# Optimization experiments

Measured on AMD Instinct MI355X. Metric: run time of the kernel, lower is better.

Reference implementation:

```python
import jax, jax.numpy as jnp
import numpy as np

N, IN_FEATS, OUT_FEATS = 8192, 512, 256


def setup_inputs() -> dict:
    key = jax.random.key(0)
    k1, k2, k3, k4 = jax.random.split(key, 4)
    feature_mat = jax.random.normal(k1, (N, IN_FEATS), dtype=jnp.float32)
    # Xavier-uniform style init for W and W2
    limW = float(np.sqrt(6.0 / (IN_FEATS + OUT_FEATS)))
    W = jax.random.uniform(k2, (IN_FEATS, OUT_FEATS), minval=-limW, maxval=limW, dtype=jnp.float32)
    limW2 = float(np.sqrt(6.0 / (2 * OUT_FEATS + 1)))
    W2 = jax.random.uniform(k3, (2 * OUT_FEATS, 1), minval=-limW2, maxval=limW2, dtype=jnp.float32)
    adj_mat = jax.random.randint(k4, (N, N), 0, 2, dtype=jnp.int32)
    return {"feature_mat": feature_mat, "W": W, "W2": W2, "adj_mat": adj_mat}


def reference(feature_mat, W, W2, adj_mat):
    out_feats = W.shape[1]
    Wh = feature_mat @ W                      # [N, F']
    Wh1 = Wh @ W2[:out_feats, :]              # [N, 1]
    Wh2 = Wh @ W2[out_feats:, :]              # [N, 1]
    e = Wh1 + Wh2.T                           # [N, N] broadcast add
    e = jnp.where(e > 0, e, 0.2 * e)          # leaky_relu(0.2)
    # NOTE: original masks with ZERO (not -inf) before softmax — faithful.
    e = jnp.where(adj_mat > 0, e, jnp.zeros((), dtype=e.dtype))
    attention = jax.nn.softmax(e, axis=1)     # row softmax over all N
    h_prime = attention @ Wh                  # [N, F']
    return jax.nn.relu(h_prime)
```

## Files before the change

kernel.cpp:

```cpp
#include <hip/hip_runtime.h>
#include <cstdint>
#include <cstddef>

#define NR 8192
#define FOUT 256
#define KIN 512
#define KSPLIT 2
#define JCHUNK (NR / KSPLIT)
#define BKJ 64
#define NSTEP (JCHUNK / BKJ)
#define IROWS 32

typedef __attribute__((ext_vector_type(8))) short bf16x8;
typedef __attribute__((ext_vector_type(4))) float f32x4;

__device__ __forceinline__ unsigned f2bf(float x) {
  unsigned u = __float_as_uint(x);
  u += 0x7fffu + ((u >> 16) & 1u);
  return u >> 16;
}
__device__ __forceinline__ float bf2f(unsigned h) {
  return __uint_as_float(h << 16);
}
__device__ __forceinline__ unsigned fkey(float x) {
  unsigned u = __float_as_uint(x);
  return (u & 0x80000000u) ? ~u : (u | 0x80000000u);
}
__device__ __forceinline__ float fkey_dec(unsigned k) {
  return __uint_as_float((k & 0x80000000u) ? (k ^ 0x80000000u) : ~k);
}

#define GLDS(g, l)                                                            \
  __builtin_amdgcn_global_load_lds(                                           \
      (const __attribute__((address_space(1))) unsigned int*)(g),             \
      (__attribute__((address_space(3))) unsigned int*)(l), 16, 0, 0)

__global__ __launch_bounds__(256) void k0_prep(const float* __restrict__ W,
                                               const float* __restrict__ W2,
                                               float* __restrict__ w1,
                                               float* __restrict__ w2,
                                               char* __restrict__ WTbf,
                                               unsigned* __restrict__ maxkey) {
  if (blockIdx.x == 0 && threadIdx.x == 0) *maxkey = 0u;
  int wv = threadIdx.x >> 6, lane = threadIdx.x & 63;
  int k = blockIdx.x * 4 + wv;
  int f4 = lane * 4;
  float4 wr = *(const float4*)(W + (size_t)k * FOUT + f4);
  float4 a = *(const float4*)(W2 + f4);
  float4 b = *(const float4*)(W2 + FOUT + f4);
  float d1 = wr.x * a.x + wr.y * a.y + wr.z * a.z + wr.w * a.w;
  float d2 = wr.x * b.x + wr.y * b.y + wr.z * b.z + wr.w * b.w;
#pragma unroll
  for (int off = 32; off; off >>= 1) {
    d1 += __shfl_xor(d1, off);
    d2 += __shfl_xor(d2, off);
  }
  if (lane == 0) {
    w1[k] = d1;
    w2[k] = d2;
  }
  int kt = k >> 5, kl = k & 31;
  float wv4[4] = {wr.x, wr.y, wr.z, wr.w};
#pragma unroll
  for (int ff = 0; ff < 4; ++ff) {
    int f = f4 + ff;
    size_t addr = (size_t)kt * 16384 + (f >> 4) * 1024 +
                  (((f & 15) | (((kl >> 3) & 3) << 4)) * 16) + (kl & 7) * 2;
    *(unsigned short*)(WTbf + addr) = (unsigned short)f2bf(wv4[ff]);
  }
}

__global__ __launch_bounds__(256) void k2_fused(
    const float* __restrict__ X, const char* __restrict__ WTbf,
    const float* __restrict__ w1, const float* __restrict__ w2,
    char* __restrict__ WhTf, float* __restrict__ Wh1, float* __restrict__ Wh2,
    unsigned* __restrict__ maxkey) {
  __shared__ char smem[2 * 18432 + 4096];
  char* buf0 = smem;
  char* buf1 = smem + 18432;
  char* wlds = smem + 2 * 18432;
  int t = threadIdx.x, wv = t >> 6, lane = t & 63;
  int jb = blockIdx.x * 32;
  int jr = t >> 3, koff = (t & 7) * 4;
  int cA = (jr & 15) | (((koff >> 3) & 3) << 4);
  int swA = cA ^ (((cA >> 4) & 3) << 2);
  int aoff = (jr >> 4) * 1024 + swA * 16 + ((koff & 4) << 1);
  int slotR = lane ^ (((lane >> 4) & 3) << 2);
  const float* xrow = X + (size_t)(jb + jr) * KIN + koff;

  {
    float2 a_ = *(const float2*)(w1 + t * 2);
    float2 b_ = *(const float2*)(w2 + t * 2);
    *(float2*)(wlds + t * 8) = a_;
    *(float2*)(wlds + 2048 + t * 8) = b_;
  }
  __syncthreads();

  float4 st0, st1, st2, st3;
  float d1 = 0.f, d2 = 0.f;
  f32x4 acc[2][4];
#pragma unroll
  for (int a = 0; a < 2; ++a)
#pragma unroll
    for (int b = 0; b < 4; ++b) acc[a][b] = (f32x4){0.f, 0.f, 0.f, 0.f};

#define K2_GLB(KT, BUFW)                                                      \
  do {                                                                        \
    const char* gs_ = WTbf + ((size_t)(KT) << 14) + (wv << 12) + lane * 16;   \
    char* ld_ = (BUFW) + 2048 + (wv << 12);                                   \
    GLDS(gs_, ld_);                                                           \
    GLDS(gs_ + 1024, ld_ + 1024);                                             \
    GLDS(gs_ + 2048, ld_ + 2048);                                             \
    GLDS(gs_ + 3072, ld_ + 3072);                                             \
  } while (0)

#define K2_LDX(KT, ST) (ST) = *(const float4*)(xrow + (KT) * 32)

#define K2_AGEN(ST, BUFW, SNUM)                                               \
  do {                                                                        \
    uint2 a_;                                                                 \
    a_.x = f2bf((ST).x) | (f2bf((ST).y) << 16);                               \
    a_.y = f2bf((ST).z) | (f2bf((ST).w) << 16);                               \
    *(uint2*)((BUFW) + aoff) = a_;                                            \
    float4 wa_ = *(const float4*)(wlds + ((SNUM)*32 + koff) * 4);             \
    float4 wb_ = *(const float4*)(wlds + 2048 + ((SNUM)*32 + koff) * 4);      \
    d1 += (ST).x * wa_.x + (ST).y * wa_.y + (ST).z * wa_.z + (ST).w * wa_.w;  \
    d2 += (ST).x * wb_.x + (ST).y * wb_.y + (ST).z * wb_.z + (ST).w * wb_.w;  \
  } while (0)

#define K2_ITER(S, BUFR, BUFW, STC, STF)                                      \
  do {                                                                        \
    int s_ = (S);                                                             \
    if (s_ + 1 < 16) K2_GLB(s_ + 1, BUFW);                                    \
    K2_LDX((s_ + 3 < 16) ? s_ + 3 : 15, STF);                                 \
    if (s_ + 1 < 16) K2_AGEN(STC, BUFW, s_ + 1);                              \
    bf16x8 a0 = *(const bf16x8*)((BUFR) + slotR * 16);                        \
    bf16x8 a1 = *(const bf16x8*)((BUFR) + 1024 + slotR * 16);                 \
    bf16x8 b0 = *(const bf16x8*)((BUFR) + 2048 + (wv * 4 + 0) * 1024 + lane * 16); \
    bf16x8 b1 = *(const bf16x8*)((BUFR) + 2048 + (wv * 4 + 1) * 1024 + lane * 16); \
    bf16x8 b2 = *(const bf16x8*)((BUFR) + 2048 + (wv * 4 + 2) * 1024 + lane * 16); \
    bf16x8 b3 = *(const bf16x8*)((BUFR) + 2048 + (wv * 4 + 3) * 1024 + lane * 16); \
    acc[0][0] = __builtin_amdgcn_mfma_f32_16x16x32_bf16(a0, b0, acc[0][0], 0, 0, 0); \
    acc[0][1] = __builtin_amdgcn_mfma_f32_16x16x32_bf16(a0, b1, acc[0][1], 0, 0, 0); \
    acc[0][2] = __builtin_amdgcn_mfma_f32_16x16x32_bf16(a0, b2, acc[0][2], 0, 0, 0); \
    acc[0][3] = __builtin_amdgcn_mfma_f32_16x16x32_bf16(a0, b3, acc[0][3], 0, 0, 0); \
    acc[1][0] = __builtin_amdgcn_mfma_f32_16x16x32_bf16(a1, b0, acc[1][0], 0, 0, 0); \
    acc[1][1] = __builtin_amdgcn_mfma_f32_16x16x32_bf16(a1, b1, acc[1][1], 0, 0, 0); \
    acc[1][2] = __builtin_amdgcn_mfma_f32_16x16x32_bf16(a1, b2, acc[1][2], 0, 0, 0); \
    acc[1][3] = __builtin_amdgcn_mfma_f32_16x16x32_bf16(a1, b3, acc[1][3], 0, 0, 0); \
    __builtin_amdgcn_sched_barrier(0);                                        \
    asm volatile("s_waitcnt vmcnt(1)");                                       \
    asm volatile("s_waitcnt lgkmcnt(0)");                                     \
    __builtin_amdgcn_s_barrier();                                             \
    __builtin_amdgcn_sched_barrier(0);                                        \
  } while (0)

  K2_GLB(0, buf0);
  K2_LDX(0, st0);
  K2_LDX(1, st1);
  K2_LDX(2, st2);
  K2_AGEN(st0, buf0, 0);
  __builtin_amdgcn_sched_barrier(0);
  asm volatile("s_waitcnt vmcnt(2)");
  asm volatile("s_waitcnt lgkmcnt(0)");
  __builtin_amdgcn_s_barrier();
  __builtin_amdgcn_sched_barrier(0);

  for (int s4 = 0; s4 < 16; s4 += 4) {
    K2_ITER(s4 + 0, buf0, buf1, st1, st3);
    K2_ITER(s4 + 1, buf1, buf0, st2, st0);
    K2_ITER(s4 + 2, buf0, buf1, st3, st1);
    K2_ITER(s4 + 3, buf1, buf0, st0, st2);
  }
#undef K2_ITER
#undef K2_AGEN
#undef K2_LDX
#undef K2_GLB

  int q = lane >> 4;
#pragma unroll
  for (int mi = 0; mi < 2; ++mi)
#pragma unroll
    for (int nn = 0; nn < 4; ++nn) {
      int u2 = wv * 4 + nn;
      int cell = (lane & 15) | ((((mi * 2) + (q >> 1)) & 3) << 4);
      uint2 v;
      v.x = f2bf(acc[mi][nn].x) | (f2bf(acc[mi][nn].y) << 16);
      v.y = f2bf(acc[mi][nn].z) | (f2bf(acc[mi][nn].w) << 16);
      *(uint2*)(buf0 + 2048 + u2 * 1024 + cell * 16 + ((q & 1) << 3)) = v;
    }
  __syncthreads();
  char* wb = WhTf + (size_t)blockIdx.x * 16384;
#pragma unroll
  for (int q2 = 0; q2 < 4; ++q2) {
    uint4 v = *(const uint4*)(buf0 + 2048 + q2 * 4096 + t * 16);
    *(uint4*)(wb + q2 * 4096 + t * 16) = v;
  }

  d1 += __shfl_xor(d1, 1);
  d1 += __shfl_xor(d1, 2);
  d1 += __shfl_xor(d1, 4);
  d2 += __shfl_xor(d2, 1);
  d2 += __shfl_xor(d2, 2);
  d2 += __shfl_xor(d2, 4);
  if ((t & 7) == 0) {
    Wh1[jb + jr] = d1;
    Wh2[jb + jr] = d2;
  }
  float mx = d2;
#pragma unroll
  for (int off = 32; off >= 8; off >>= 1) mx = fmaxf(mx, __shfl_xor(mx, off));
  __shared__ float red[4];
  if (lane == 0) red[wv] = mx;
  __syncthreads();
  if (t == 0) {
    float bm = fmaxf(fmaxf(red[0], red[1]), fmaxf(red[2], red[3]));
    atomicMax(maxkey, fkey(bm));
  }
}

__device__ __forceinline__ uint2 hv4(int4 aq, float4 wq, float wh1, float m,
                                     float enm, float& z) {
  float s0 = wh1 + wq.x, s1 = wh1 + wq.y, s2 = wh1 + wq.z, s3 = wh1 + wq.w;
  s0 = s0 > 0.f ? s0 : 0.2f * s0;
  s1 = s1 > 0.f ? s1 : 0.2f * s1;
  s2 = s2 > 0.f ? s2 : 0.2f * s2;
  s3 = s3 > 0.f ? s3 : 0.2f * s3;
  float w0 = aq.x > 0 ? __expf(s0 - m) : enm;
  float w1 = aq.y > 0 ? __expf(s1 - m) : enm;
  float w2 = aq.z > 0 ? __expf(s2 - m) : enm;
  float w3 = aq.w > 0 ? __expf(s3 - m) : enm;
  unsigned h0 = f2bf(w0), h1 = f2bf(w1), h2 = f2bf(w2), h3 = f2bf(w3);
  z += bf2f(h0) + bf2f(h1) + bf2f(h2) + bf2f(h3);
  uint2 r;
  r.x = h0 | (h1 << 16);
  r.y = h2 | (h3 << 16);
  return r;
}

__global__ __launch_bounds__(512, 4) void k3_attn(
    const int* __restrict__ adj, const char* __restrict__ WhTf,
    const float* __restrict__ Wh1, const float* __restrict__ Wh2,
    const unsigned* __restrict__ maxptr, float* __restrict__ PVp,
    float* __restrict__ Zp) {
  __shared__ char smem[24576];
  char* abuf0 = smem;
  char* abuf1 = smem + 4096;
  char* wlds = smem + 8192;
  int t = threadIdx.x, wv = t >> 6, lane = t & 63;
  int kc = blockIdx.x & 1;
  int ib = blockIdx.x >> 1;
  int ibase = ib * IROWS;
  int jbch = kc * JCHUNK;
  int r0 = t >> 4;
  int jg = (t & 15) * 4;
  int iglob = ibase + r0;
  float maxwh2 = fkey_dec(*maxptr);
  float wh1 = Wh1[iglob];
  float m = fmaxf(0.f, wh1 + maxwh2);
  float enm = __expf(-m);
  int cA = (r0 & 15) | (((jg >> 3) & 3) << 4);
  int swA = cA ^ (((cA >> 4) & 3) << 2);
  int aoff = ((r0 >> 4) * 2 + (jg >> 5)) * 1024 + swA * 16 + ((jg & 4) << 1);
  int slotR = lane ^ (((lane >> 4) & 3) << 2);
  const int* adjrow = adj + ((size_t)iglob << 13) + jbch + jg;
  const char* bbase = WhTf + ((size_t)(kc * 128) << 14) + (size_t)(wv * 2) * 1024 +
                      (size_t)lane * 16;
  const char* wl = wlds + ((t & 15) << 4);

  {
    const float* wp = Wh2 + jbch + t * 8;
    *(float4*)(wlds + t * 32) = *(const float4*)(wp);
    *(float4*)(wlds + t * 32 + 16) = *(const float4*)(wp + 4);
  }
  __syncthreads();

  int4 st0, st1, st2, st3;
  bf16x8 bA0, bA1, bA2, bA3, bB0, bB1, bB2, bB3;
  f32x4 acc[2][2];
#pragma unroll
  for (int a = 0; a < 2; ++a)
#pragma unroll
    for (int b = 0; b < 2; ++b) acc[a][b] = (f32x4){0.f, 0.f, 0.f, 0.f};
  float zacc = 0.f;

#define K3_LDB(S, B0, B1, B2, B3)                                             \
  do {                                                                        \
    int sc_ = (S) < NSTEP ? (S) : NSTEP - 1;                                  \
    const char* bp_ = bbase + (size_t)(2 * sc_) * 16384;                      \
    B0 = *(const bf16x8*)(bp_);                                               \
    B1 = *(const bf16x8*)(bp_ + 1024);                                        \
    B2 = *(const bf16x8*)(bp_ + 16384);                                       \
    B3 = *(const bf16x8*)(bp_ + 16384 + 1024);                                \
  } while (0)

#define K3_LDA(S, ST)                                                         \
  do {                                                                        \
    int sc_ = (S) < NSTEP ? (S) : NSTEP - 1;                                  \
    ST = *(const int4*)(adjrow + sc_ * BKJ);                                  \
  } while (0)

#define K3_ITER(S, AR, AW, BC0, BC1, BC2, BC3, BF0, BF1, BF2, BF3, STC, STF,  \
                DO_HV)                                                        \
  do {                                                                        \
    int s_ = (S);                                                             \
    K3_LDB(s_ + 1, BF0, BF1, BF2, BF3);                                       \
    K3_LDA(s_ + 4, STF);                                                      \
    if (DO_HV) {                                                              \
      float4 wq_ = *(const float4*)(wl + (s_ + 1) * 256);                     \
      uint2 a_ = hv4(STC, wq_, wh1, m, enm, zacc);                            \
      *(uint2*)((AW) + aoff) = a_;                                            \
    }                                                                         \
    bf16x8 a00 = *(const bf16x8*)((AR) + 0 * 1024 + slotR * 16);              \
    bf16x8 a10 = *(const bf16x8*)((AR) + 2 * 1024 + slotR * 16);              \
    bf16x8 a01 = *(const bf16x8*)((AR) + 1 * 1024 + slotR * 16);              \
    bf16x8 a11 = *(const bf16x8*)((AR) + 3 * 1024 + slotR * 16);              \
    acc[0][0] = __builtin_amdgcn_mfma_f32_16x16x32_bf16(a00, BC0, acc[0][0], 0, 0, 0); \
    acc[0][1] = __builtin_amdgcn_mfma_f32_16x16x32_bf16(a00, BC1, acc[0][1], 0, 0, 0); \
    acc[1][0] = __builtin_amdgcn_mfma_f32_16x16x32_bf16(a10, BC0, acc[1][0], 0, 0, 0); \
    acc[1][1] = __builtin_amdgcn_mfma_f32_16x16x32_bf16(a10, BC1, acc[1][1], 0, 0, 0); \
    acc[0][0] = __builtin_amdgcn_mfma_f32_16x16x32_bf16(a01, BC2, acc[0][0], 0, 0, 0); \
    acc[0][1] = __builtin_amdgcn_mfma_f32_16x16x32_bf16(a01, BC3, acc[0][1], 0, 0, 0); \
    acc[1][0] = __builtin_amdgcn_mfma_f32_16x16x32_bf16(a11, BC2, acc[1][0], 0, 0, 0); \
    acc[1][1] = __builtin_amdgcn_mfma_f32_16x16x32_bf16(a11, BC3, acc[1][1], 0, 0, 0); \
    __builtin_amdgcn_sched_barrier(0);                                        \
    asm volatile("s_waitcnt lgkmcnt(0)" ::: "memory");                        \
    __builtin_amdgcn_s_barrier();                                             \
    __builtin_amdgcn_sched_barrier(0);                                        \
  } while (0)

  K3_LDB(0, bA0, bA1, bA2, bA3);
  int4 adj0;
  K3_LDA(0, adj0);
  K3_LDA(1, st1);
  K3_LDA(2, st2);
  K3_LDA(3, st3);
  {
    float4 wq0 = *(const float4*)(wl);
    uint2 a0 = hv4(adj0, wq0, wh1, m, enm, zacc);
    *(uint2*)(abuf0 + aoff) = a0;
  }
  __builtin_amdgcn_sched_barrier(0);
  asm volatile("s_waitcnt lgkmcnt(0)" ::: "memory");
  __builtin_amdgcn_s_barrier();
  __builtin_amdgcn_sched_barrier(0);

  for (int s4 = 0; s4 < NSTEP - 4; s4 += 4) {
    K3_ITER(s4 + 0, abuf0, abuf1, bA0, bA1, bA2, bA3, bB0, bB1, bB2, bB3, st1, st0, 1);
    K3_ITER(s4 + 1, abuf1, abuf0, bB0, bB1, bB2, bB3, bA0, bA1, bA2, bA3, st2, st1, 1);
    K3_ITER(s4 + 2, abuf0, abuf1, bA0, bA1, bA2, bA3, bB0, bB1, bB2, bB3, st3, st2, 1);
    K3_ITER(s4 + 3, abuf1, abuf0, bB0, bB1, bB2, bB3, bA0, bA1, bA2, bA3, st0, st3, 1);
  }
  K3_ITER(NSTEP - 4, abuf0, abuf1, bA0, bA1, bA2, bA3, bB0, bB1, bB2, bB3, st1, st0, 1);
  K3_ITER(NSTEP - 3, abuf1, abuf0, bB0, bB1, bB2, bB3, bA0, bA1, bA2, bA3, st2, st1, 1);
  K3_ITER(NSTEP - 2, abuf0, abuf1, bA0, bA1, bA2, bA3, bB0, bB1, bB2, bB3, st3, st2, 1);
  K3_ITER(NSTEP - 1, abuf1, abuf0, bB0, bB1, bB2, bB3, bA0, bA1, bA2, bA3, st0, st3, 0);
#undef K3_ITER
#undef K3_LDA
#undef K3_LDB

  zacc += __shfl_xor(zacc, 1);
  zacc += __shfl_xor(zacc, 2);
  zacc += __shfl_xor(zacc, 4);
  zacc += __shfl_xor(zacc, 8);
  if ((t & 15) == 0) Zp[(size_t)kc * NR + iglob] = zacc;
#pragma unroll
  for (int rf = 0; rf < 2; ++rf)
#pragma unroll
    for (int un = 0; un < 2; ++un) {
      int f = wv * 32 + un * 16 + (lane & 15);
      int row0 = ibase + rf * 16 + ((lane >> 4) << 2);
      size_t base = ((size_t)kc * NR + row0) * FOUT + f;
      PVp[base + 0 * FOUT] = acc[rf][un].x;
      PVp[base + 1 * FOUT] = acc[rf][un].y;
      PVp[base + 2 * FOUT] = acc[rf][un].z;
      PVp[base + 3 * FOUT] = acc[rf][un].w;
    }
}

__global__ __launch_bounds__(256) void k4_reduce(const float* __restrict__ PVp,
                                                 const float* __restrict__ Zp,
                                                 float* __restrict__ out) {
  int tid = blockIdx.x * 256 + threadIdx.x;
  int i = tid >> 6;
  int f4 = (tid & 63) * 4;
  float z = Zp[i] + Zp[NR + i];
  float4 p0 = *(const float4*)(PVp + (size_t)i * FOUT + f4);
  float4 p1 = *(const float4*)(PVp + ((size_t)NR + i) * FOUT + f4);
  float inv = 1.f / z;
  float4 r;
  r.x = fmaxf((p0.x + p1.x) * inv, 0.f);
  r.y = fmaxf((p0.y + p1.y) * inv, 0.f);
  r.z = fmaxf((p0.z + p1.z) * inv, 0.f);
  r.w = fmaxf((p0.w + p1.w) * inv, 0.f);
  *(float4*)(out + (size_t)i * FOUT + f4) = r;
}

extern "C" void kernel_launch(void* const* d_in, const int* in_sizes, int n_in,
                              void* d_out, int out_size, void* d_ws,
                              size_t ws_size, hipStream_t stream) {
  const float* X = (const float*)d_in[0];
  const float* W = (const float*)d_in[1];
  const float* W2 = (const float*)d_in[2];
  const int* adj = (const int*)d_in[3];
  float* out = (float*)d_out;
  char* ws = (char*)d_ws;

  const size_t WHT_OFF = 0;
  const size_t WTBF_OFF = (size_t)4 * 1024 * 1024;
  const size_t W1_OFF = WTBF_OFF + 256 * 1024;
  const size_t W2V_OFF = W1_OFF + 2048;
  const size_t WH1_OFF = W2V_OFF + 2048;
  const size_t WH2_OFF = WH1_OFF + 32768;
  const size_t MXK_OFF = WH2_OFF + 32768;
  const size_t ZP_OFF = MXK_OFF + 256;
  const size_t PV_OFF = ZP_OFF + (size_t)KSPLIT * NR * 4;

  char* WhTf = ws + WHT_OFF;
  char* WTbf = ws + WTBF_OFF;
  float* w1 = (float*)(ws + W1_OFF);
  float* w2 = (float*)(ws + W2V_OFF);
  float* Wh1 = (float*)(ws + WH1_OFF);
  float* Wh2 = (float*)(ws + WH2_OFF);
  unsigned* maxkey = (unsigned*)(ws + MXK_OFF);
  float* Zp = (float*)(ws + ZP_OFF);
  float* PVp = (float*)(ws + PV_OFF);

  k0_prep<<<128, 256, 0, stream>>>(W, W2, w1, w2, WTbf, maxkey);
  k2_fused<<<256, 256, 0, stream>>>(X, WTbf, w1, w2, WhTf, Wh1, Wh2, maxkey);
  k3_attn<<<512, 512, 0, stream>>>(adj, WhTf, Wh1, Wh2, maxkey, PVp, Zp);
  k4_reduce<<<2048, 256, 0, stream>>>(PVp, Zp, out);
}
```

Measured before the change: 130.4 us.

## Double row tile and split columns four ways in attention kernel

Raises the attention block's row tile from 32 to 64 rows and the column split from 2 to 4 chunks. Each thread now builds 8 probability values per step, and each wave runs 4x2 MFMA tiles per step, so every bf16 Wh B-fragment loaded from global memory is reused across twice as many rows. The adjacency prefetch depth shrinks from 4 stages to 2. The reduce kernel now sums four partial products, which doubles the partial-output traffic written and read.

```diff
diff --git a/kernel.cpp b/kernel.cpp
--- a/kernel.cpp
+++ b/kernel.cpp
@@ -5,11 +5,11 @@
 #define NR 8192
 #define FOUT 256
 #define KIN 512
-#define KSPLIT 2
+#define KSPLIT 4
 #define JCHUNK (NR / KSPLIT)
 #define BKJ 64
 #define NSTEP (JCHUNK / BKJ)
-#define IROWS 32
+#define IROWS 64
 
 typedef __attribute__((ext_vector_type(8))) short bf16x8;
 typedef __attribute__((ext_vector_type(4))) float f32x4;
@@ -237,6 +237,12 @@
   r.y = h2 | (h3 << 16);
   return r;
 }
+__device__ __forceinline__ uint4 hv8(int4 a0, int4 a1, float4 w0, float4 w1,
+                                     float wh1, float m, float enm, float& z) {
+  uint2 r0 = hv4(a0, w0, wh1, m, enm, z);
+  uint2 r1 = hv4(a1, w1, wh1, m, enm, z);
+  return (uint4){r0.x, r0.y, r1.x, r1.y};
+}
 
 __global__ __launch_bounds__(512, 4) void k3_attn(
     const int* __restrict__ adj, const char* __restrict__ WhTf,
@@ -245,41 +251,38 @@
     float* __restrict__ Zp) {
   __shared__ char smem[24576];
   char* abuf0 = smem;
-  char* abuf1 = smem + 4096;
-  char* wlds = smem + 8192;
+  char* abuf1 = smem + 8192;
+  char* wlds = smem + 16384;
   int t = threadIdx.x, wv = t >> 6, lane = t & 63;
-  int kc = blockIdx.x & 1;
-  int ib = blockIdx.x >> 1;
+  int kc = blockIdx.x & 3;
+  int ib = blockIdx.x >> 2;
   int ibase = ib * IROWS;
   int jbch = kc * JCHUNK;
-  int r0 = t >> 4;
-  int jg = (t & 15) * 4;
+  int r0 = t >> 3;
+  int j8 = (t & 7) * 8;
   int iglob = ibase + r0;
   float maxwh2 = fkey_dec(*maxptr);
   float wh1 = Wh1[iglob];
   float m = fmaxf(0.f, wh1 + maxwh2);
   float enm = __expf(-m);
-  int cA = (r0 & 15) | (((jg >> 3) & 3) << 4);
+  int unitA = (r0 >> 4) * 2 + (j8 >> 5);
+  int cA = (r0 & 15) | (((j8 & 31) >> 3) << 4);
   int swA = cA ^ (((cA >> 4) & 3) << 2);
-  int aoff = ((r0 >> 4) * 2 + (jg >> 5)) * 1024 + swA * 16 + ((jg & 4) << 1);
+  int aoff = unitA * 1024 + swA * 16;
   int slotR = lane ^ (((lane >> 4) & 3) << 2);
-  const int* adjrow = adj + ((size_t)iglob << 13) + jbch + jg;
-  const char* bbase = WhTf + ((size_t)(kc * 128) << 14) + (size_t)(wv * 2) * 1024 +
-                      (size_t)lane * 16;
-  const char* wl = wlds + ((t & 15) << 4);
-
-  {
-    const float* wp = Wh2 + jbch + t * 8;
-    *(float4*)(wlds + t * 32) = *(const float4*)(wp);
-    *(float4*)(wlds + t * 32 + 16) = *(const float4*)(wp + 4);
-  }
+  const int* adjrow = adj + ((size_t)iglob << 13) + jbch + j8;
+  const char* bbase = WhTf + ((size_t)(kc * 64) << 14) +
+                      (size_t)(wv * 2) * 1024 + (size_t)lane * 16;
+  const char* wl = wlds + j8 * 4;
+
+  *(float4*)(wlds + t * 16) = *(const float4*)(Wh2 + jbch + t * 4);
   __syncthreads();
 
-  int4 st0, st1, st2, st3;
   bf16x8 bA0, bA1, bA2, bA3, bB0, bB1, bB2, bB3;
-  f32x4 acc[2][2];
-#pragma unroll
-  for (int a = 0; a < 2; ++a)
+  int4 st0_a, st0_b, st1_a, st1_b;
+  f32x4 acc[4][2];
+#pragma unroll
+  for (int a = 0; a < 4; ++a)
 #pragma unroll
     for (int b = 0; b < 2; ++b) acc[a][b] = (f32x4){0.f, 0.f, 0.f, 0.f};
   float zacc = 0.f;
@@ -297,32 +300,30 @@
 #define K3_LDA(S, ST)                                                         \
   do {                                                                        \
     int sc_ = (S) < NSTEP ? (S) : NSTEP - 1;                                  \
-    ST = *(const int4*)(adjrow + sc_ * BKJ);                                  \
-  } while (0)
-
-#define K3_ITER(S, AR, AW, BC0, BC1, BC2, BC3, BF0, BF1, BF2, BF3, STC, STF,  \
-                DO_HV)                                                        \
+    ST##_a = *(const int4*)(adjrow + sc_ * BKJ);                              \
+    ST##_b = *(const int4*)(adjrow + sc_ * BKJ + 4);                          \
+  } while (0)
+
+#define K3_ITER(S, AR, AW, BC0, BC1, BC2, BC3, BF0, BF1, BF2, BF3, STC, DO_HV) \
   do {                                                                        \
     int s_ = (S);                                                             \
     K3_LDB(s_ + 1, BF0, BF1, BF2, BF3);                                       \
-    K3_LDA(s_ + 4, STF);                                                      \
     if (DO_HV) {                                                              \
-      float4 wq_ = *(const float4*)(wl + (s_ + 1) * 256);                     \
-      uint2 a_ = hv4(STC, wq_, wh1, m, enm, zacc);                            \
-      *(uint2*)((AW) + aoff) = a_;                                            \
+      float4 wq0_ = *(const float4*)(wl + (s_ + 1) * 256);                    \
+      float4 wq1_ = *(const float4*)(wl + (s_ + 1) * 256 + 16);               \
+      uint4 a_ = hv8(STC##_a, STC##_b, wq0_, wq1_, wh1, m, enm, zacc);        \
+      *(uint4*)((AW) + aoff) = a_;                                            \
     }                                                                         \
-    bf16x8 a00 = *(const bf16x8*)((AR) + 0 * 1024 + slotR * 16);              \
-    bf16x8 a10 = *(const bf16x8*)((AR) + 2 * 1024 + slotR * 16);              \
-    bf16x8 a01 = *(const bf16x8*)((AR) + 1 * 1024 + slotR * 16);              \
-    bf16x8 a11 = *(const bf16x8*)((AR) + 3 * 1024 + slotR * 16);              \
-    acc[0][0] = __builtin_amdgcn_mfma_f32_16x16x32_bf16(a00, BC0, acc[0][0], 0, 0, 0); \
-    acc[0][1] = __builtin_amdgcn_mfma_f32_16x16x32_bf16(a00, BC1, acc[0][1], 0, 0, 0); \
-    acc[1][0] = __builtin_amdgcn_mfma_f32_16x16x32_bf16(a10, BC0, acc[1][0], 0, 0, 0); \
-    acc[1][1] = __builtin_amdgcn_mfma_f32_16x16x32_bf16(a10, BC1, acc[1][1], 0, 0, 0); \
-    acc[0][0] = __builtin_amdgcn_mfma_f32_16x16x32_bf16(a01, BC2, acc[0][0], 0, 0, 0); \
-    acc[0][1] = __builtin_amdgcn_mfma_f32_16x16x32_bf16(a01, BC3, acc[0][1], 0, 0, 0); \
-    acc[1][0] = __builtin_amdgcn_mfma_f32_16x16x32_bf16(a11, BC2, acc[1][0], 0, 0, 0); \
-    acc[1][1] = __builtin_amdgcn_mfma_f32_16x16x32_bf16(a11, BC3, acc[1][1], 0, 0, 0); \
+    K3_LDA(s_ + 3, STC);                                                      \
+    _Pragma("unroll")                                                         \
+    for (int rf_ = 0; rf_ < 4; ++rf_) {                                       \
+      bf16x8 ak0_ = *(const bf16x8*)((AR) + (rf_ * 2 + 0) * 1024 + slotR * 16); \
+      bf16x8 ak1_ = *(const bf16x8*)((AR) + (rf_ * 2 + 1) * 1024 + slotR * 16); \
+      acc[rf_][0] = __builtin_amdgcn_mfma_f32_16x16x32_bf16(ak0_, BC0, acc[rf_][0], 0, 0, 0); \
+      acc[rf_][1] = __builtin_amdgcn_mfma_f32_16x16x32_bf16(ak0_, BC1, acc[rf_][1], 0, 0, 0); \
+      acc[rf_][0] = __builtin_amdgcn_mfma_f32_16x16x32_bf16(ak1_, BC2, acc[rf_][0], 0, 0, 0); \
+      acc[rf_][1] = __builtin_amdgcn_mfma_f32_16x16x32_bf16(ak1_, BC3, acc[rf_][1], 0, 0, 0); \
+    }                                                                         \
     __builtin_amdgcn_sched_barrier(0);                                        \
     asm volatile("s_waitcnt lgkmcnt(0)" ::: "memory");                        \
     __builtin_amdgcn_s_barrier();                                             \
@@ -330,31 +331,27 @@
   } while (0)
 
   K3_LDB(0, bA0, bA1, bA2, bA3);
-  int4 adj0;
-  K3_LDA(0, adj0);
+  int4 adj0a = *(const int4*)(adjrow);
+  int4 adj0b = *(const int4*)(adjrow + 4);
   K3_LDA(1, st1);
-  K3_LDA(2, st2);
-  K3_LDA(3, st3);
+  K3_LDA(2, st0);
   {
     float4 wq0 = *(const float4*)(wl);
-    uint2 a0 = hv4(adj0, wq0, wh1, m, enm, zacc);
-    *(uint2*)(abuf0 + aoff) = a0;
+    float4 wq1 = *(const float4*)(wl + 16);
+    uint4 a0 = hv8(adj0a, adj0b, wq0, wq1, wh1, m, enm, zacc);
+    *(uint4*)(abuf0 + aoff) = a0;
   }
   __builtin_amdgcn_sched_barrier(0);
   asm volatile("s_waitcnt lgkmcnt(0)" ::: "memory");
   __builtin_amdgcn_s_barrier();
   __builtin_amdgcn_sched_barrier(0);
 
-  for (int s4 = 0; s4 < NSTEP - 4; s4 += 4) {
-    K3_ITER(s4 + 0, abuf0, abuf1, bA0, bA1, bA2, bA3, bB0, bB1, bB2, bB3, st1, st0, 1);
-    K3_ITER(s4 + 1, abuf1, abuf0, bB0, bB1, bB2, bB3, bA0, bA1, bA2, bA3, st2, st1, 1);
-    K3_ITER(s4 + 2, abuf0, abuf1, bA0, bA1, bA2, bA3, bB0, bB1, bB2, bB3, st3, st2, 1);
-    K3_ITER(s4 + 3, abuf1, abuf0, bB0, bB1, bB2, bB3, bA0, bA1, bA2, bA3, st0, st3, 1);
-  }
-  K3_ITER(NSTEP - 4, abuf0, abuf1, bA0, bA1, bA2, bA3, bB0, bB1, bB2, bB3, st1, st0, 1);
-  K3_ITER(NSTEP - 3, abuf1, abuf0, bB0, bB1, bB2, bB3, bA0, bA1, bA2, bA3, st2, st1, 1);
-  K3_ITER(NSTEP - 2, abuf0, abuf1, bA0, bA1, bA2, bA3, bB0, bB1, bB2, bB3, st3, st2, 1);
-  K3_ITER(NSTEP - 1, abuf1, abuf0, bB0, bB1, bB2, bB3, bA0, bA1, bA2, bA3, st0, st3, 0);
+  for (int s2 = 0; s2 < NSTEP - 2; s2 += 2) {
+    K3_ITER(s2 + 0, abuf0, abuf1, bA0, bA1, bA2, bA3, bB0, bB1, bB2, bB3, st1, 1);
+    K3_ITER(s2 + 1, abuf1, abuf0, bB0, bB1, bB2, bB3, bA0, bA1, bA2, bA3, st0, 1);
+  }
+  K3_ITER(NSTEP - 2, abuf0, abuf1, bA0, bA1, bA2, bA3, bB0, bB1, bB2, bB3, st1, 1);
+  K3_ITER(NSTEP - 1, abuf1, abuf0, bB0, bB1, bB2, bB3, bA0, bA1, bA2, bA3, st0, 0);
 #undef K3_ITER
 #undef K3_LDA
 #undef K3_LDB
@@ -362,13 +359,12 @@
   zacc += __shfl_xor(zacc, 1);
   zacc += __shfl_xor(zacc, 2);
   zacc += __shfl_xor(zacc, 4);
-  zacc += __shfl_xor(zacc, 8);
-  if ((t & 15) == 0) Zp[(size_t)kc * NR + iglob] = zacc;
-#pragma unroll
-  for (int rf = 0; rf < 2; ++rf)
+  if ((t & 7) == 0) Zp[(size_t)kc * NR + iglob] = zacc;
+#pragma unroll
+  for (int rf = 0; rf < 4; ++rf)
 #pragma unroll
     for (int un = 0; un < 2; ++un) {
-      int f = wv * 32 + un * 16 + (lane & 15);
+      int f = (wv * 2 + un) * 16 + (lane & 15);
       int row0 = ibase + rf * 16 + ((lane >> 4) << 2);
       size_t base = ((size_t)kc * NR + row0) * FOUT + f;
       PVp[base + 0 * FOUT] = acc[rf][un].x;
@@ -384,15 +380,22 @@
   int tid = blockIdx.x * 256 + threadIdx.x;
   int i = tid >> 6;
   int f4 = (tid & 63) * 4;
-  float z = Zp[i] + Zp[NR + i];
-  float4 p0 = *(const float4*)(PVp + (size_t)i * FOUT + f4);
-  float4 p1 = *(const float4*)(PVp + ((size_t)NR + i) * FOUT + f4);
+  float z = Zp[i] + Zp[NR + i] + Zp[2 * NR + i] + Zp[3 * NR + i];
+  float4 a = {0.f, 0.f, 0.f, 0.f};
+#pragma unroll
+  for (int c = 0; c < KSPLIT; ++c) {
+    float4 p = *(const float4*)(PVp + ((size_t)c * NR + i) * FOUT + f4);
+    a.x += p.x;
+    a.y += p.y;
+    a.z += p.z;
+    a.w += p.w;
+  }
   float inv = 1.f / z;
   float4 r;
-  r.x = fmaxf((p0.x + p1.x) * inv, 0.f);
-  r.y = fmaxf((p0.y + p1.y) * inv, 0.f);
-  r.z = fmaxf((p0.z + p1.z) * inv, 0.f);
-  r.w = fmaxf((p0.w + p1.w) * inv, 0.f);
+  r.x = fmaxf(a.x * inv, 0.f);
+  r.y = fmaxf(a.y * inv, 0.f);
+  r.z = fmaxf(a.z * inv, 0.f);
+  r.w = fmaxf(a.w * inv, 0.f);
   *(float4*)(out + (size_t)i * FOUT + f4) = r;
 }
 
```

Measured after the change: 118.3 us. 1.1x faster.
